# Optimization experiments

Hardware: AMD Instinct MI355X
Metric: run time of the kernel (lower is better)

## Reference

```python
import jax, jax.numpy as jnp
import numpy as np

C = 256          # in_dim
DQK = C // 16    # query/key channels after 1x1 conv


def setup_inputs() -> dict:
    key = jax.random.key(0)
    ks = jax.random.split(key, 10)
    B, W, H = 8, 64, 64
    s = 0.02
    return {
        "x1": jax.random.normal(ks[0], (B, C, W, H), jnp.float32),
        "x2": jax.random.normal(ks[1], (B, C, W, H), jnp.float32),
        "Wq": jax.random.normal(ks[2], (DQK, 2 * C), jnp.float32) * s,
        "bq": jnp.zeros((DQK,), jnp.float32),
        "Wk": jax.random.normal(ks[3], (DQK, 2 * C), jnp.float32) * s,
        "bk": jnp.zeros((DQK,), jnp.float32),
        "Wv1": jax.random.normal(ks[4], (C, C), jnp.float32) * s,
        "bv1": jnp.zeros((C,), jnp.float32),
        "Wv2": jax.random.normal(ks[5], (C, C), jnp.float32) * s,
        "bv2": jnp.zeros((C,), jnp.float32),
    }


def reference(x1, x2, Wq, bq, Wk, bk, Wv1, bv1, Wv2, bv2):
    B, c, W, H = x1.shape
    N = W * H
    x = jnp.concatenate([x1, x2], axis=1)            # [B, 2C, W, H]
    xf = x.reshape(B, 2 * c, N)                      # flatten spatial
    # 1x1 convs == channel matmuls
    q = jnp.einsum('dc,bcn->bnd', Wq, xf) + bq       # [B, N, DQK]
    k = jnp.einsum('dc,bcn->bdn', Wk, xf) + bk[None, :, None]  # [B, DQK, N]
    energy = jnp.einsum('bnd,bdm->bnm', q, k)        # [B, N, N]
    attention = jax.nn.softmax(energy, axis=-1)
    x1f = x1.reshape(B, c, N)
    x2f = x2.reshape(B, c, N)
    v1 = jnp.einsum('oc,bcn->bon', Wv1, x1f) + bv1[None, :, None]
    v2 = jnp.einsum('oc,bcn->bon', Wv2, x2f) + bv2[None, :, None]
    # bmm(value, attention^T): out[b,c,n] = sum_m v[b,c,m] * attention[b,n,m]
    out1 = jnp.einsum('bcm,bnm->bcn', v1, attention).reshape(B, c, W, H) + x1
    out2 = jnp.einsum('bcm,bnm->bcn', v2, attention).reshape(B, c, W, H) + x2
    return out1, out2, attention
```

## Files before the change

kernel.cpp:

```cpp
#include <hip/hip_runtime.h>
#include <hip/hip_bf16.h>

#define B_ 8
#define C_ 256
#define N_ 4096
#define D_ 16
#define TWO_C 512

typedef __bf16 bf16x8 __attribute__((ext_vector_type(8)));
typedef __bf16 bf16x4 __attribute__((ext_vector_type(4)));
typedef float f32x4 __attribute__((ext_vector_type(4)));
typedef unsigned short u16x4 __attribute__((ext_vector_type(4)));

static __device__ __forceinline__ unsigned short f2bf_rtn(float f) {
    unsigned int u = __builtin_bit_cast(unsigned int, f);
    u += 0x7fffu + ((u >> 16) & 1u);
    return (unsigned short)(u >> 16);
}

__device__ __forceinline__ void gld16(const void* g, void* l) {
    __builtin_amdgcn_global_load_lds(
        (const __attribute__((address_space(1))) unsigned int*)g,
        (__attribute__((address_space(3))) unsigned int*)l, 16, 0, 0);
}

#define MF(K, Q) __builtin_amdgcn_mfma_f32_16x16x32_bf16((K), (Q), zerov, 0, 0, 0)

__global__ __launch_bounds__(256) void wconv(
    const float* __restrict__ Wv1, const float* __restrict__ Wv2,
    unsigned short* __restrict__ Wbf)
{
    const int i = blockIdx.x * 256 + threadIdx.x;
    f32x4 a = ((const f32x4*)Wv1)[i];
    f32x4 b = ((const f32x4*)Wv2)[i];
    u16x4 ua = { f2bf_rtn(a[0]), f2bf_rtn(a[1]), f2bf_rtn(a[2]), f2bf_rtn(a[3]) };
    u16x4 ub = { f2bf_rtn(b[0]), f2bf_rtn(b[1]), f2bf_rtn(b[2]), f2bf_rtn(b[3]) };
    ((u16x4*)Wbf)[i] = ua;
    ((u16x4*)Wbf)[16384 + i] = ub;
}

__global__ __launch_bounds__(256) void qk_part(
    const float* __restrict__ x1, const float* __restrict__ x2,
    const float* __restrict__ Wq, const float* __restrict__ Wk,
    float* __restrict__ pq, float* __restrict__ pk,
    unsigned short* __restrict__ xbfT)
{
    const int tid = threadIdx.x;
    const int bid = blockIdx.x;
    const int ch = bid & 3;
    const int nt = (bid >> 2) & 15;
    const int b  = bid >> 6;
    const int n  = nt * 256 + tid;

    const float* xs  = (ch < 2) ? x1 : x2;
    const int xoff = (ch & 1) * 128;
    const int wcol = ch * 128;

    const float* px = xs + ((size_t)b * C_ + xoff) * N_ + n;
    unsigned short* xT = xbfT + ((size_t)b * N_ + n) * TWO_C + wcol;

    float aq[D_], ak[D_];
#pragma unroll
    for (int d = 0; d < D_; ++d) { aq[d] = 0.f; ak[d] = 0.f; }

    for (int c8 = 0; c8 < 16; ++c8) {
        unsigned short xb[8];
#pragma unroll
        for (int j = 0; j < 8; ++j) {
            const int c = c8 * 8 + j;
            float xv = px[(size_t)c * N_];
            xb[j] = f2bf_rtn(xv);
#pragma unroll
            for (int d = 0; d < D_; ++d) {
                aq[d] += Wq[d * TWO_C + wcol + c] * xv;
                ak[d] += Wk[d * TWO_C + wcol + c] * xv;
            }
        }
        u16x4 lo = { xb[0], xb[1], xb[2], xb[3] };
        u16x4 hi = { xb[4], xb[5], xb[6], xb[7] };
        *(u16x4*)(xT + c8 * 8)     = lo;
        *(u16x4*)(xT + c8 * 8 + 4) = hi;
    }

    f32x4* q4 = (f32x4*)pq + (size_t)ch * B_ * N_ * 4 + ((size_t)b * N_ + n) * 4;
    f32x4* k4 = (f32x4*)pk + (size_t)ch * B_ * N_ * 4 + ((size_t)b * N_ + n) * 4;
#pragma unroll
    for (int j = 0; j < 4; ++j) {
        f32x4 tq = { aq[4*j], aq[4*j+1], aq[4*j+2], aq[4*j+3] };
        f32x4 tk = { ak[4*j], ak[4*j+1], ak[4*j+2], ak[4*j+3] };
        q4[j] = tq;
        k4[j] = tk;
    }
}

__global__ __launch_bounds__(256) void qk_reduce(
    const float* __restrict__ pq, const float* __restrict__ pk,
    const float* __restrict__ bq, const float* __restrict__ bk,
    unsigned short* __restrict__ qbf, unsigned short* __restrict__ kbf)
{
    const int tg = blockIdx.x * 256 + threadIdx.x;
    const int row = tg >> 2;
    const int d4  = tg & 3;
    const f32x4* pq4 = (const f32x4*)pq;
    const f32x4* pk4 = (const f32x4*)pk;
    f32x4 q = ((const f32x4*)bq)[d4];
    f32x4 k = ((const f32x4*)bk)[d4];
    const size_t stride = (size_t)B_ * N_ * 4;
#pragma unroll
    for (int ch = 0; ch < 4; ++ch) {
        q += pq4[ch * stride + tg];
        k += pk4[ch * stride + tg];
    }
    u16x4 qo = { f2bf_rtn(q[0]), f2bf_rtn(q[1]), f2bf_rtn(q[2]), f2bf_rtn(q[3]) };
    u16x4 ko = { f2bf_rtn(k[0]), f2bf_rtn(k[1]), f2bf_rtn(k[2]), f2bf_rtn(k[3]) };
    u16x4 z  = { 0, 0, 0, 0 };
    *(u16x4*)(qbf + (size_t)row * 32 + d4 * 4)      = qo;
    *(u16x4*)(qbf + (size_t)row * 32 + 16 + d4 * 4) = z;
    *(u16x4*)(kbf + (size_t)row * 32 + d4 * 4)      = ko;
    *(u16x4*)(kbf + (size_t)row * 32 + 16 + d4 * 4) = z;
}

__global__ __launch_bounds__(256) void v_mfma(
    const unsigned short* __restrict__ Wbf,
    const unsigned short* __restrict__ xbfT,
    const float* __restrict__ bv1, const float* __restrict__ bv2,
    unsigned short* __restrict__ vstack)
{
    const int tid  = threadIdx.x;
    const int lane = tid & 63;
    const int wid  = tid >> 6;
    const int bid  = blockIdx.x;
    const int b    = bid >> 7;
    const int half = (bid >> 6) & 1;
    const int n0   = (bid & 63) * 64;
    const int col  = lane & 15;
    const int grp  = lane >> 4;
    const int koff = grp * 8;

    const unsigned short* pa[4];
    const unsigned short* pb[4];
#pragma unroll
    for (int ai = 0; ai < 4; ++ai)
        pa[ai] = Wbf + (size_t)(half * 256 + wid * 64 + ai * 16 + col) * 256 + koff;
#pragma unroll
    for (int bj = 0; bj < 4; ++bj)
        pb[bj] = xbfT + ((size_t)b * N_ + n0 + bj * 16 + col) * TWO_C + half * 256 + koff;

    f32x4 acc[4][4];
#pragma unroll
    for (int ai = 0; ai < 4; ++ai)
#pragma unroll
        for (int bj = 0; bj < 4; ++bj)
            acc[ai][bj] = (f32x4){0.f, 0.f, 0.f, 0.f};

#pragma unroll
    for (int s = 0; s < 8; ++s) {
        bf16x8 af[4], bfr[4];
#pragma unroll
        for (int ai = 0; ai < 4; ++ai) af[ai] = *(const bf16x8*)(pa[ai] + s * 32);
#pragma unroll
        for (int bj = 0; bj < 4; ++bj) bfr[bj] = *(const bf16x8*)(pb[bj] + s * 32);
#pragma unroll
        for (int ai = 0; ai < 4; ++ai)
#pragma unroll
            for (int bj = 0; bj < 4; ++bj)
                acc[ai][bj] = __builtin_amdgcn_mfma_f32_16x16x32_bf16(
                    af[ai], bfr[bj], acc[ai][bj], 0, 0, 0);
    }

    const float* bias = half ? bv2 : bv1;
#pragma unroll
    for (int ai = 0; ai < 4; ++ai) {
        const int cb = wid * 64 + ai * 16 + grp * 4;
#pragma unroll
        for (int r = 0; r < 4; ++r) {
            const float bv = bias[cb + r];
            unsigned short* vr = vstack + ((size_t)b * 512 + half * 256 + cb + r) * N_;
#pragma unroll
            for (int bj = 0; bj < 4; ++bj)
                vr[n0 + bj * 16 + col] = f2bf_rtn(acc[ai][bj][r] + bv);
        }
    }
}

__global__ __launch_bounds__(512) void fused_pv(
    const unsigned short* __restrict__ qbf,
    const unsigned short* __restrict__ kbf,
    const unsigned short* __restrict__ vstack,
    const float* __restrict__ x1, const float* __restrict__ x2,
    float* __restrict__ out1, float* __restrict__ out2,
    float* __restrict__ att)
{
    __shared__ unsigned short Asm[2][256 * 32];
    __shared__ unsigned short Bsm[2][256 * 32];
    __shared__ float sinv[256];

    const int tid  = threadIdx.x;
    const int lane = tid & 63;
    const int wid  = tid >> 6;
    const int wr   = wid >> 2;
    const int wc   = wid & 3;
    const int col  = lane & 15;
    const int grp  = lane >> 4;

    const int bid  = blockIdx.x;
    const int orig = (bid & 7) * 32 + (bid >> 3);
    const int nt = orig & 15;
    const int ct = (orig >> 4) & 1;
    const int b  = orig >> 5;
    const int n0 = nt * 256;

    const f32x4 zerov = {0.f, 0.f, 0.f, 0.f};

    const bf16x8 qf0 = *(const bf16x8*)(qbf + ((size_t)b * N_ + n0 + wid * 32 + col) * 32 + grp * 8);
    const bf16x8 qf1 = *(const bf16x8*)(qbf + ((size_t)b * N_ + n0 + wid * 32 + 16 + col) * 32 + grp * 8);

    const unsigned short* kbase = kbf + ((size_t)b * N_ + col) * 32 + grp * 8;

    const unsigned short* Vb = vstack + ((size_t)b * 512 + ct * 256) * N_;
    const int q1 = tid + 512;
    const unsigned short* pa0 = Vb + (size_t)(tid >> 2) * N_ + (((tid & 3) ^ ((tid >> 2) & 3)) * 8);
    const unsigned short* pa1 = Vb + (size_t)(q1 >> 2) * N_ + (((q1 & 3) ^ ((q1 >> 2) & 3)) * 8);

    const int nl0 = wid * 32 + col;
    const int bwA = nl0 * 64 + ((((grp >> 1)) ^ (col & 3)) << 4) + (grp & 1) * 8;
    const int bwB = bwA ^ 32;

    const int raBase = (wr * 128 + col) * 64 + ((grp ^ (col & 3)) << 4);
    const int rbBase = (wc * 64  + col) * 64 + ((grp ^ (col & 3)) << 4);

    f32x4 acc[8][4];
#pragma unroll
    for (int ai = 0; ai < 8; ++ai)
#pragma unroll
        for (int bj = 0; bj < 4; ++bj)
            acc[ai][bj] = zerov;

    float rsum0 = 0.f, rsum1 = 0.f;

#define EMITB(E, RS, BASE, OFF) do {                                          \
    float p0 = __expf((E)[0]), p1 = __expf((E)[1]);                           \
    float p2 = __expf((E)[2]), p3 = __expf((E)[3]);                           \
    RS += (p0 + p1) + (p2 + p3);                                              \
    bf16x4 pkv = { (__bf16)p0, (__bf16)p1, (__bf16)p2, (__bf16)p3 };          \
    *(bf16x4*)((char*)(BASE) + (OFF)) = pkv;                                  \
} while (0)

    gld16(pa0, &Asm[0][tid * 8]);
    gld16(pa1, &Asm[0][tid * 8 + 4096]);
    pa0 += 32; pa1 += 32;
    bf16x8 kA0 = *(const bf16x8*)kbase;
    bf16x8 kA1 = *(const bf16x8*)(kbase + 512);
    const unsigned short* kp = kbase + 1024;
    bf16x8 kB0, kB1;
    {
        f32x4 e00 = MF(kA0, qf0);
        f32x4 e01 = MF(kA1, qf0);
        f32x4 e10 = MF(kA0, qf1);
        f32x4 e11 = MF(kA1, qf1);
        kB0 = *(const bf16x8*)kp;
        kB1 = *(const bf16x8*)(kp + 512);
        kp += 1024;
        EMITB(e00, rsum0, &Bsm[0][0], bwA);
        EMITB(e01, rsum0, &Bsm[0][0], bwB);
        EMITB(e10, rsum1, &Bsm[0][0], bwA + 1024);
        EMITB(e11, rsum1, &Bsm[0][0], bwB + 1024);
    }
    __syncthreads();

    auto step = [&](const unsigned short* AsCur, unsigned short* AsNxt,
                    const unsigned short* BsCur, unsigned short* BsNxt,
                    const bf16x8& kc0, const bf16x8& kc1,
                    bf16x8& kn0, bf16x8& kn1, bool doNext) {
        bf16x8 bfr[4], af0[4], af1[4];
#pragma unroll
        for (int bj = 0; bj < 4; ++bj)
            bfr[bj] = *(const bf16x8*)((const char*)BsCur + rbBase + bj * 1024);
#pragma unroll
        for (int ai = 0; ai < 4; ++ai)
            af0[ai] = *(const bf16x8*)((const char*)AsCur + raBase + ai * 1024);
        if (doNext) {
            gld16(pa0, AsNxt + tid * 8);
            gld16(pa1, AsNxt + tid * 8 + 4096);
            pa0 += 32; pa1 += 32;
        }
        if (doNext) {
            f32x4 e00 = MF(kc0, qf0);
            f32x4 e01 = MF(kc1, qf0);
            f32x4 e10 = MF(kc0, qf1);
            f32x4 e11 = MF(kc1, qf1);
            kn0 = *(const bf16x8*)kp;
            kn1 = *(const bf16x8*)(kp + 512);
            kp += 1024;
            EMITB(e00, rsum0, BsNxt, bwA);
            EMITB(e01, rsum0, BsNxt, bwB);
            EMITB(e10, rsum1, BsNxt, bwA + 1024);
            EMITB(e11, rsum1, BsNxt, bwB + 1024);
        }
#pragma unroll
        for (int ai = 0; ai < 4; ++ai)
#pragma unroll
            for (int bj = 0; bj < 4; ++bj)
                acc[ai][bj] = __builtin_amdgcn_mfma_f32_16x16x32_bf16(
                    af0[ai], bfr[bj], acc[ai][bj], 0, 0, 0);
#pragma unroll
        for (int ai = 0; ai < 4; ++ai)
            af1[ai] = *(const bf16x8*)((const char*)AsCur + raBase + (4 + ai) * 1024);
#pragma unroll
        for (int ai = 0; ai < 4; ++ai)
#pragma unroll
            for (int bj = 0; bj < 4; ++bj)
                acc[4 + ai][bj] = __builtin_amdgcn_mfma_f32_16x16x32_bf16(
                    af1[ai], bfr[bj], acc[4 + ai][bj], 0, 0, 0);
        if (doNext) {
            asm volatile("s_waitcnt vmcnt(0) lgkmcnt(0)" ::: "memory");
            __builtin_amdgcn_s_barrier();
            __builtin_amdgcn_sched_barrier(0);
        }
    };

    for (int tt = 0; tt < 64; ++tt) {
        step(&Asm[0][0], &Asm[1][0], &Bsm[0][0], &Bsm[1][0], kB0, kB1, kA0, kA1, true);
        step(&Asm[1][0], &Asm[0][0], &Bsm[1][0], &Bsm[0][0], kA0, kA1, kB0, kB1, tt < 63);
    }

    rsum0 += __shfl_xor(rsum0, 16); rsum0 += __shfl_xor(rsum0, 32);
    rsum1 += __shfl_xor(rsum1, 16); rsum1 += __shfl_xor(rsum1, 32);
    const float inv0 = 1.f / rsum0;
    const float inv1 = 1.f / rsum1;
    if (lane < 16) {
        sinv[wid * 32 + lane]      = inv0;
        sinv[wid * 32 + 16 + lane] = inv1;
    }
    __syncthreads();

    float* outp     = ct ? out2 : out1;
    const float* xp = ct ? x2 : x1;
    float sc[4];
#pragma unroll
    for (int bj = 0; bj < 4; ++bj) sc[bj] = sinv[wc * 64 + bj * 16 + col];
#pragma unroll
    for (int ai = 0; ai < 8; ++ai) {
        const int c_l = wr * 128 + ai * 16 + grp * 4;
#pragma unroll
        for (int bj = 0; bj < 4; ++bj) {
            const int n = n0 + wc * 64 + bj * 16 + col;
#pragma unroll
            for (int r = 0; r < 4; ++r) {
                const size_t idx = ((size_t)b * C_ + c_l + r) * N_ + n;
                outp[idx] = acc[ai][bj][r] * sc[bj] + xp[idx];
            }
        }
    }

    const unsigned short* kp2 = kbase + (size_t)(ct * 2048) * 32;
    float* ar0 = att + (size_t)b * N_ * N_ + (size_t)(n0 + wid * 32 + col) * N_;
    float* ar1 = ar0 + (size_t)16 * N_;

#define WRA(E, ROW, MOFF, INV) do {                                           \
    f32x4 pv = { __expf((E)[0]) * (INV), __expf((E)[1]) * (INV),              \
                 __expf((E)[2]) * (INV), __expf((E)[3]) * (INV) };            \
    *(f32x4*)((ROW) + (MOFF)) = pv;                                           \
} while (0)

    for (int s = 0; s < 64; ++s) {
        const int m0 = ct * 2048 + s * 32;
        bf16x8 k0 = *(const bf16x8*)kp2;
        bf16x8 k1 = *(const bf16x8*)(kp2 + 512);
        kp2 += 1024;
        f32x4 e00 = MF(k0, qf0);
        f32x4 e01 = MF(k1, qf0);
        f32x4 e10 = MF(k0, qf1);
        f32x4 e11 = MF(k1, qf1);
        WRA(e00, ar0, m0 + grp * 4,      inv0);
        WRA(e01, ar0, m0 + 16 + grp * 4, inv0);
        WRA(e10, ar1, m0 + grp * 4,      inv1);
        WRA(e11, ar1, m0 + 16 + grp * 4, inv1);
    }
#undef EMITB
#undef WRA
}

extern "C" void kernel_launch(void* const* d_in, const int* in_sizes, int n_in,
                              void* d_out, int out_size, void* d_ws, size_t ws_size,
                              hipStream_t stream)
{
    const float* x1  = (const float*)d_in[0];
    const float* x2  = (const float*)d_in[1];
    const float* Wq  = (const float*)d_in[2];
    const float* bq  = (const float*)d_in[3];
    const float* Wk  = (const float*)d_in[4];
    const float* bk  = (const float*)d_in[5];
    const float* Wv1 = (const float*)d_in[6];
    const float* bv1 = (const float*)d_in[7];
    const float* Wv2 = (const float*)d_in[8];
    const float* bv2 = (const float*)d_in[9];

    float* out  = (float*)d_out;
    float* out1 = out;
    float* out2 = out + (size_t)B_ * C_ * N_;
    float* att  = out + 2 * (size_t)B_ * C_ * N_;

    unsigned short* xbfT = (unsigned short*)att;

    char* ws = (char*)d_ws;
    unsigned short* qbf = (unsigned short*)ws;
    unsigned short* kbf = (unsigned short*)(ws + (size_t)2 * 1024 * 1024);
    unsigned short* vstack = (unsigned short*)(ws + (size_t)4 * 1024 * 1024);
    float* pq = (float*)(ws + (size_t)36 * 1024 * 1024);
    float* pk = (float*)(ws + (size_t)44 * 1024 * 1024);
    unsigned short* Wbf = (unsigned short*)(ws + (size_t)52 * 1024 * 1024);

    wconv<<<64, 256, 0, stream>>>(Wv1, Wv2, Wbf);
    qk_part<<<B_ * 16 * 4, 256, 0, stream>>>(x1, x2, Wq, Wk, pq, pk, xbfT);
    qk_reduce<<<(B_ * N_ * 4) / 256, 256, 0, stream>>>(pq, pk, bq, bk, qbf, kbf);
    v_mfma<<<B_ * 2 * 64, 256, 0, stream>>>(Wbf, xbfT, bv1, bv2, vstack);
    fused_pv<<<256, 512, 0, stream>>>(qbf, kbf, vstack, x1, x2, out1, out2, att);
}
```

Baseline: 445.8 us.

## Precompute softmax row sums first, then stream attention writes inside the PV loop

```diff
diff --git a/kernel.cpp b/kernel.cpp
--- a/kernel.cpp
+++ b/kernel.cpp
@@ -22,6 +22,11 @@
     __builtin_amdgcn_global_load_lds(
         (const __attribute__((address_space(1))) unsigned int*)g,
         (__attribute__((address_space(3))) unsigned int*)l, 16, 0, 0);
+}
+
+__device__ __forceinline__ f32x4 expv(f32x4 e) {
+    f32x4 r = { __expf(e[0]), __expf(e[1]), __expf(e[2]), __expf(e[3]) };
+    return r;
 }
 
 #define MF(K, Q) __builtin_amdgcn_mfma_f32_16x16x32_bf16((K), (Q), zerov, 0, 0, 0)
@@ -217,113 +222,24 @@
 
     const unsigned short* kbase = kbf + ((size_t)b * N_ + col) * 32 + grp * 8;
 
-    const unsigned short* Vb = vstack + ((size_t)b * 512 + ct * 256) * N_;
-    const int q1 = tid + 512;
-    const unsigned short* pa0 = Vb + (size_t)(tid >> 2) * N_ + (((tid & 3) ^ ((tid >> 2) & 3)) * 8);
-    const unsigned short* pa1 = Vb + (size_t)(q1 >> 2) * N_ + (((q1 & 3) ^ ((q1 >> 2) & 3)) * 8);
-
-    const int nl0 = wid * 32 + col;
-    const int bwA = nl0 * 64 + ((((grp >> 1)) ^ (col & 3)) << 4) + (grp & 1) * 8;
-    const int bwB = bwA ^ 32;
-
-    const int raBase = (wr * 128 + col) * 64 + ((grp ^ (col & 3)) << 4);
-    const int rbBase = (wc * 64  + col) * 64 + ((grp ^ (col & 3)) << 4);
-
-    f32x4 acc[8][4];
-#pragma unroll
-    for (int ai = 0; ai < 8; ++ai)
-#pragma unroll
-        for (int bj = 0; bj < 4; ++bj)
-            acc[ai][bj] = zerov;
-
     float rsum0 = 0.f, rsum1 = 0.f;
-
-#define EMITB(E, RS, BASE, OFF) do {                                          \
-    float p0 = __expf((E)[0]), p1 = __expf((E)[1]);                           \
-    float p2 = __expf((E)[2]), p3 = __expf((E)[3]);                           \
-    RS += (p0 + p1) + (p2 + p3);                                              \
-    bf16x4 pkv = { (__bf16)p0, (__bf16)p1, (__bf16)p2, (__bf16)p3 };          \
-    *(bf16x4*)((char*)(BASE) + (OFF)) = pkv;                                  \
-} while (0)
-
-    gld16(pa0, &Asm[0][tid * 8]);
-    gld16(pa1, &Asm[0][tid * 8 + 4096]);
-    pa0 += 32; pa1 += 32;
-    bf16x8 kA0 = *(const bf16x8*)kbase;
-    bf16x8 kA1 = *(const bf16x8*)(kbase + 512);
-    const unsigned short* kp = kbase + 1024;
-    bf16x8 kB0, kB1;
     {
-        f32x4 e00 = MF(kA0, qf0);
-        f32x4 e01 = MF(kA1, qf0);
-        f32x4 e10 = MF(kA0, qf1);
-        f32x4 e11 = MF(kA1, qf1);
-        kB0 = *(const bf16x8*)kp;
-        kB1 = *(const bf16x8*)(kp + 512);
-        kp += 1024;
-        EMITB(e00, rsum0, &Bsm[0][0], bwA);
-        EMITB(e01, rsum0, &Bsm[0][0], bwB);
-        EMITB(e10, rsum1, &Bsm[0][0], bwA + 1024);
-        EMITB(e11, rsum1, &Bsm[0][0], bwB + 1024);
-    }
-    __syncthreads();
-
-    auto step = [&](const unsigned short* AsCur, unsigned short* AsNxt,
-                    const unsigned short* BsCur, unsigned short* BsNxt,
-                    const bf16x8& kc0, const bf16x8& kc1,
-                    bf16x8& kn0, bf16x8& kn1, bool doNext) {
-        bf16x8 bfr[4], af0[4], af1[4];
-#pragma unroll
-        for (int bj = 0; bj < 4; ++bj)
-            bfr[bj] = *(const bf16x8*)((const char*)BsCur + rbBase + bj * 1024);
-#pragma unroll
-        for (int ai = 0; ai < 4; ++ai)
-            af0[ai] = *(const bf16x8*)((const char*)AsCur + raBase + ai * 1024);
-        if (doNext) {
-            gld16(pa0, AsNxt + tid * 8);
-            gld16(pa1, AsNxt + tid * 8 + 4096);
-            pa0 += 32; pa1 += 32;
-        }
-        if (doNext) {
-            f32x4 e00 = MF(kc0, qf0);
-            f32x4 e01 = MF(kc1, qf0);
-            f32x4 e10 = MF(kc0, qf1);
-            f32x4 e11 = MF(kc1, qf1);
-            kn0 = *(const bf16x8*)kp;
-            kn1 = *(const bf16x8*)(kp + 512);
-            kp += 1024;
-            EMITB(e00, rsum0, BsNxt, bwA);
-            EMITB(e01, rsum0, BsNxt, bwB);
-            EMITB(e10, rsum1, BsNxt, bwA + 1024);
-            EMITB(e11, rsum1, BsNxt, bwB + 1024);
-        }
-#pragma unroll
-        for (int ai = 0; ai < 4; ++ai)
-#pragma unroll
-            for (int bj = 0; bj < 4; ++bj)
-                acc[ai][bj] = __builtin_amdgcn_mfma_f32_16x16x32_bf16(
-                    af0[ai], bfr[bj], acc[ai][bj], 0, 0, 0);
-#pragma unroll
-        for (int ai = 0; ai < 4; ++ai)
-            af1[ai] = *(const bf16x8*)((const char*)AsCur + raBase + (4 + ai) * 1024);
-#pragma unroll
-        for (int ai = 0; ai < 4; ++ai)
-#pragma unroll
-            for (int bj = 0; bj < 4; ++bj)
-                acc[4 + ai][bj] = __builtin_amdgcn_mfma_f32_16x16x32_bf16(
-                    af1[ai], bfr[bj], acc[4 + ai][bj], 0, 0, 0);
-        if (doNext) {
-            asm volatile("s_waitcnt vmcnt(0) lgkmcnt(0)" ::: "memory");
-            __builtin_amdgcn_s_barrier();
-            __builtin_amdgcn_sched_barrier(0);
-        }
-    };
-
-    for (int tt = 0; tt < 64; ++tt) {
-        step(&Asm[0][0], &Asm[1][0], &Bsm[0][0], &Bsm[1][0], kB0, kB1, kA0, kA1, true);
-        step(&Asm[1][0], &Asm[0][0], &Bsm[1][0], &Bsm[0][0], kA0, kA1, kB0, kB1, tt < 63);
-    }
-
+        const unsigned short* kq = kbase;
+#pragma unroll 2
+        for (int T = 0; T < 128; ++T) {
+            bf16x8 k0 = *(const bf16x8*)kq;
+            bf16x8 k1 = *(const bf16x8*)(kq + 512);
+            kq += 1024;
+            f32x4 p00 = expv(MF(k0, qf0));
+            f32x4 p01 = expv(MF(k1, qf0));
+            f32x4 p10 = expv(MF(k0, qf1));
+            f32x4 p11 = expv(MF(k1, qf1));
+            rsum0 += (p00[0] + p00[1]) + (p00[2] + p00[3])
+                   + (p01[0] + p01[1]) + (p01[2] + p01[3]);
+            rsum1 += (p10[0] + p10[1]) + (p10[2] + p10[3])
+                   + (p11[0] + p11[1]) + (p11[2] + p11[3]);
+        }
+    }
     rsum0 += __shfl_xor(rsum0, 16); rsum0 += __shfl_xor(rsum0, 32);
     rsum1 += __shfl_xor(rsum1, 16); rsum1 += __shfl_xor(rsum1, 32);
     const float inv0 = 1.f / rsum0;
@@ -332,8 +248,125 @@
         sinv[wid * 32 + lane]      = inv0;
         sinv[wid * 32 + 16 + lane] = inv1;
     }
+
+    const unsigned short* Vb = vstack + ((size_t)b * 512 + ct * 256) * N_;
+    const int q1 = tid + 512;
+    const unsigned short* pa0 = Vb + (size_t)(tid >> 2) * N_ + (((tid & 3) ^ ((tid >> 2) & 3)) * 8);
+    const unsigned short* pa1 = Vb + (size_t)(q1 >> 2) * N_ + (((q1 & 3) ^ ((q1 >> 2) & 3)) * 8);
+
+    const int nl0 = wid * 32 + col;
+    const int bwA = nl0 * 64 + ((((grp >> 1)) ^ (col & 3)) << 4) + (grp & 1) * 8;
+    const int bwB = bwA ^ 32;
+
+    const int raBase = (wr * 128 + col) * 64 + ((grp ^ (col & 3)) << 4);
+    const int rbBase = (wc * 64  + col) * 64 + ((grp ^ (col & 3)) << 4);
+
+    float* ars0 = att + (size_t)b * N_ * N_ + (size_t)(n0 + wid * 32 + col) * N_
+                + ct * 16 + grp * 4;
+    float* ars1 = ars0 + (size_t)16 * N_;
+
+    f32x4 acc[8][4];
+#pragma unroll
+    for (int ai = 0; ai < 8; ++ai)
+#pragma unroll
+        for (int bj = 0; bj < 4; ++bj)
+            acc[ai][bj] = zerov;
+
+#define PACKB(P, BASE, OFF) do {                                              \
+    bf16x4 pkv = { (__bf16)(P)[0], (__bf16)(P)[1],                            \
+                   (__bf16)(P)[2], (__bf16)(P)[3] };                          \
+    *(bf16x4*)((char*)(BASE) + (OFF)) = pkv;                                  \
+} while (0)
+
+    gld16(pa0, &Asm[0][tid * 8]);
+    gld16(pa1, &Asm[0][tid * 8 + 4096]);
+    pa0 += 32; pa1 += 32;
+    __builtin_amdgcn_sched_barrier(0);
+    bf16x8 kA0 = *(const bf16x8*)kbase;
+    bf16x8 kA1 = *(const bf16x8*)(kbase + 512);
+    const unsigned short* kp = kbase + 1024;
+    bf16x8 kB0, kB1;
+    {
+        f32x4 p00 = expv(MF(kA0, qf0));
+        f32x4 p01 = expv(MF(kA1, qf0));
+        f32x4 p10 = expv(MF(kA0, qf1));
+        f32x4 p11 = expv(MF(kA1, qf1));
+        kB0 = *(const bf16x8*)kp;
+        kB1 = *(const bf16x8*)(kp + 512);
+        kp += 1024;
+        PACKB(p00, &Bsm[0][0], bwA);
+        PACKB(p01, &Bsm[0][0], bwB);
+        PACKB(p10, &Bsm[0][0], bwA + 1024);
+        PACKB(p11, &Bsm[0][0], bwB + 1024);
+        *(f32x4*)ars0 = (ct ? p01 : p00) * inv0;
+        *(f32x4*)ars1 = (ct ? p11 : p10) * inv1;
+    }
+    asm volatile("s_waitcnt vmcnt(4) lgkmcnt(0)" ::: "memory");
+    __builtin_amdgcn_s_barrier();
+    __builtin_amdgcn_sched_barrier(0);
+
+    auto step = [&](const unsigned short* AsCur, unsigned short* AsNxt,
+                    const unsigned short* BsCur, unsigned short* BsNxt,
+                    const bf16x8& kc0, const bf16x8& kc1,
+                    bf16x8& kn0, bf16x8& kn1, int T, bool doNext) {
+        bf16x8 bfr[4], af0[4], af1[4];
+#pragma unroll
+        for (int bj = 0; bj < 4; ++bj)
+            bfr[bj] = *(const bf16x8*)((const char*)BsCur + rbBase + bj * 1024);
+#pragma unroll
+        for (int ai = 0; ai < 4; ++ai)
+            af0[ai] = *(const bf16x8*)((const char*)AsCur + raBase + ai * 1024);
+        if (doNext) {
+            gld16(pa0, AsNxt + tid * 8);
+            gld16(pa1, AsNxt + tid * 8 + 4096);
+            pa0 += 32; pa1 += 32;
+        }
+        __builtin_amdgcn_sched_barrier(0);
+        if (doNext) {
+            f32x4 p00 = expv(MF(kc0, qf0));
+            f32x4 p01 = expv(MF(kc1, qf0));
+            f32x4 p10 = expv(MF(kc0, qf1));
+            f32x4 p11 = expv(MF(kc1, qf1));
+            kn0 = *(const bf16x8*)kp;
+            kn1 = *(const bf16x8*)(kp + 512);
+            kp += 1024;
+            PACKB(p00, BsNxt, bwA);
+            PACKB(p01, BsNxt, bwB);
+            PACKB(p10, BsNxt, bwA + 1024);
+            PACKB(p11, BsNxt, bwB + 1024);
+            *(f32x4*)(ars0 + (size_t)T * 32) = (ct ? p01 : p00) * inv0;
+            *(f32x4*)(ars1 + (size_t)T * 32) = (ct ? p11 : p10) * inv1;
+        }
+#pragma unroll
+        for (int ai = 0; ai < 4; ++ai)
+#pragma unroll
+            for (int bj = 0; bj < 4; ++bj)
+                acc[ai][bj] = __builtin_amdgcn_mfma_f32_16x16x32_bf16(
+                    af0[ai], bfr[bj], acc[ai][bj], 0, 0, 0);
+#pragma unroll
+        for (int ai = 0; ai < 4; ++ai)
+            af1[ai] = *(const bf16x8*)((const char*)AsCur + raBase + (4 + ai) * 1024);
+#pragma unroll
+        for (int ai = 0; ai < 4; ++ai)
+#pragma unroll
+            for (int bj = 0; bj < 4; ++bj)
+                acc[4 + ai][bj] = __builtin_amdgcn_mfma_f32_16x16x32_bf16(
+                    af1[ai], bfr[bj], acc[4 + ai][bj], 0, 0, 0);
+        if (doNext) {
+            asm volatile("s_waitcnt vmcnt(4) lgkmcnt(0)" ::: "memory");
+            __builtin_amdgcn_s_barrier();
+            __builtin_amdgcn_sched_barrier(0);
+        }
+    };
+
+    for (int tt = 0; tt < 64; ++tt) {
+        step(&Asm[0][0], &Asm[1][0], &Bsm[0][0], &Bsm[1][0], kB0, kB1, kA0, kA1,
+             2 * tt + 1, true);
+        step(&Asm[1][0], &Asm[0][0], &Bsm[1][0], &Bsm[0][0], kA0, kA1, kB0, kB1,
+             2 * tt + 2, tt < 63);
+    }
+
     __syncthreads();
-
     float* outp     = ct ? out2 : out1;
     const float* xp = ct ? x2 : x1;
     float sc[4];
@@ -352,33 +385,7 @@
             }
         }
     }
-
-    const unsigned short* kp2 = kbase + (size_t)(ct * 2048) * 32;
-    float* ar0 = att + (size_t)b * N_ * N_ + (size_t)(n0 + wid * 32 + col) * N_;
-    float* ar1 = ar0 + (size_t)16 * N_;
-
-#define WRA(E, ROW, MOFF, INV) do {                                           \
-    f32x4 pv = { __expf((E)[0]) * (INV), __expf((E)[1]) * (INV),              \
-                 __expf((E)[2]) * (INV), __expf((E)[3]) * (INV) };            \
-    *(f32x4*)((ROW) + (MOFF)) = pv;                                           \
-} while (0)
-
-    for (int s = 0; s < 64; ++s) {
-        const int m0 = ct * 2048 + s * 32;
-        bf16x8 k0 = *(const bf16x8*)kp2;
-        bf16x8 k1 = *(const bf16x8*)(kp2 + 512);
-        kp2 += 1024;
-        f32x4 e00 = MF(k0, qf0);
-        f32x4 e01 = MF(k1, qf0);
-        f32x4 e10 = MF(k0, qf1);
-        f32x4 e11 = MF(k1, qf1);
-        WRA(e00, ar0, m0 + grp * 4,      inv0);
-        WRA(e01, ar0, m0 + 16 + grp * 4, inv0);
-        WRA(e10, ar1, m0 + grp * 4,      inv1);
-        WRA(e11, ar1, m0 + 16 + grp * 4, inv1);
-    }
-#undef EMITB
-#undef WRA
+#undef PACKB
 }
 
 extern "C" void kernel_launch(void* const* d_in, const int* in_sizes, int n_in,
```

Measured after the change: 483.4 us. 1.08x slower.
